# Optimization experiments

Measured on AMD Instinct MI355X. Metric: run time of the kernel, lower is better.

The kernel has to match this reference:

```python
import jax, jax.numpy as jnp
import numpy as np

RADIUS = 1.0
NSAMPLE = 32


def setup_inputs() -> dict:
    key = jax.random.key(0)
    k1, k2, k3, k4, k5 = jax.random.split(key, 5)
    B, Nb, M, K, C = 2, 2048, 64, 216, 32
    N = B * Nb
    # points in a 20m cube
    xyz = jax.random.uniform(k1, (N, 3), dtype=jnp.float32) * 20.0
    xyz_batch_cnt = jnp.array([Nb, Nb], dtype=jnp.int32)
    # rois: [x,y,z,dx,dy,dz,ry]
    ctr = jax.random.uniform(k2, (B, M, 3), dtype=jnp.float32) * 20.0
    dims = 1.0 + jax.random.uniform(k3, (B, M, 3), dtype=jnp.float32) * 2.0
    ry = jax.random.uniform(k4, (B, M, 1), dtype=jnp.float32) * 6.28
    rois = jnp.concatenate([ctr, dims, ry], axis=-1)
    # 6x6x6 grid points jittered around each roi center
    off = (jax.random.uniform(k5, (B, M, K, 3), dtype=jnp.float32) - 0.5) * 3.0
    new_xyz = ctr[:, :, None, :] + off
    features = jax.random.normal(jax.random.fold_in(key, 7), (N, C), dtype=jnp.float32)
    return {"xyz": xyz, "xyz_batch_cnt": xyz_batch_cnt, "new_xyz": new_xyz,
            "rois": rois, "features": features}


def _query_and_group(xyz, new_xyz, rois, features, B, Nb):
    """Ball query -> ragged compaction (padded to L=N*nsample) -> gather."""
    M, K = new_xyz.shape[1], new_xyz.shape[2]
    MK = M * K
    N = B * Nb
    L = N * NSAMPLE
    xyz_b = xyz.reshape(B, Nb, 3)
    grid = new_xyz.reshape(B, MK, 3)
    # squared distances point -> grid center, (B, Nb, MK)
    d2 = jnp.sum((xyz_b[:, :, None, :] - grid[:, None, :, :]) ** 2, axis=-1)
    # roi bounding sphere: center rois[:,:,:3], radius ||dims||_2 (the `ball` tensor)
    ctr = rois[:, :, :3]
    r2 = jnp.sum(rois[:, :, 3:6] ** 2, axis=-1)          # (B, M)
    d2b = jnp.sum((xyz_b[:, :, None, :] - ctr[:, None, :, :]) ** 2, axis=-1)  # (B,Nb,M)
    in_ball = (d2b <= r2[:, None, :])[:, :, :, None]      # (B,Nb,M,1)
    mask = (d2 <= RADIUS * RADIUS) & jnp.broadcast_to(in_ball, (B, Nb, M, K)).reshape(B, Nb, MK)
    # first-NSAMPLE-in-order selection per point (matches kernel iteration order)
    rank = jnp.cumsum(mask.astype(jnp.int32), axis=2) - 1
    cols = jnp.where(mask & (rank < NSAMPLE), rank, NSAMPLE)  # NSAMPLE = OOB -> dropped
    rows = jnp.broadcast_to(
        jnp.arange(B, dtype=jnp.int32)[:, None, None] * Nb
        + jnp.arange(Nb, dtype=jnp.int32)[None, :, None], (B, Nb, MK))
    flat_idx = jnp.broadcast_to(
        jnp.arange(B, dtype=jnp.int32)[:, None, None] * MK
        + jnp.arange(MK, dtype=jnp.int32)[None, None, :], (B, Nb, MK))
    ball_idx = jnp.full((N, NSAMPLE), -1, dtype=jnp.int32)
    ball_idx = ball_idx.at[rows.reshape(-1), cols.reshape(-1)].set(
        flat_idx.reshape(-1), mode="drop")
    # BallIndice: cumsum compaction of valid (point_idx, grid_idx) pairs, row-major
    valid = (ball_idx > -1).reshape(-1)                  # (L,)
    pos = jnp.cumsum(valid.astype(jnp.int32)) - 1
    pos_w = jnp.where(valid, pos, L)                     # invalid -> OOB -> dropped
    row_ids = jnp.broadcast_to(
        jnp.arange(N, dtype=jnp.int32)[:, None], (N, NSAMPLE)).reshape(-1)
    set_indices = jnp.zeros((L,), jnp.int32).at[pos_w].set(row_ids, mode="drop")
    set_new_indices = jnp.zeros((L,), jnp.int32).at[pos_w].set(
        ball_idx.reshape(-1), mode="drop")
    nind = jnp.sum(valid.astype(jnp.int32))
    vm = (jnp.arange(L) < nind)[:, None].astype(features.dtype)  # padding mask
    # GatherFeature (padded slots zeroed, matching new_zeros semantics)
    group_xyz = xyz[set_indices] * vm
    group_new_xyz = new_xyz.reshape(-1, 3)[set_new_indices] * vm
    group_feat = features[set_indices] * vm
    group_features = jnp.concatenate([group_xyz - group_new_xyz, group_feat], axis=1)
    return group_features, set_new_indices


def reference(xyz, xyz_batch_cnt, new_xyz, rois, features):
    B = xyz_batch_cnt.shape[0]
    Nb = xyz.shape[0] // B
    return _query_and_group(xyz, new_xyz, rois, features, B, Nb)
```

## Files before the change

kernel.cpp:

```cpp
#include <hip/hip_runtime.h>


#pragma clang fp contract(off)

typedef unsigned long long u64;

#define MAXN 4096

__global__ __launch_bounds__(256) void count_kernel(
    const float* __restrict__ xyz, const float* __restrict__ new_xyz,
    const float* __restrict__ rois, int* __restrict__ counts,
    int* __restrict__ ballidx, float* __restrict__ out_all,
    int N, int Nb, int M, int K, int nsample, int totalOut)
{
    __shared__ int plist[4][64];
    const int wave = threadIdx.x >> 6;
    const int lane = threadIdx.x & 63;
    const int r = blockIdx.x * 4 + wave;
    const u64 laneLt = (1ull << lane) - 1ull;

    {
        const int gtid = blockIdx.x * 256 + threadIdx.x;
        const int gthreads = gridDim.x * 256;
        for (int i = gtid; i < totalOut; i += gthreads) out_all[i] = 0.0f;
    }

    if (r >= N) return;

    const int b  = r / Nb;
    const float px = xyz[3 * r + 0];
    const float py = xyz[3 * r + 1];
    const float pz = xyz[3 * r + 2];

    bool pass = false;
    if (lane < M) {
        const float* rp = rois + (size_t)(b * M + lane) * 7;
        const float dx = rp[3], dy = rp[4], dz = rp[5];
        const float r2 = (dx * dx + dy * dy) + dz * dz;
        const float ex = px - rp[0], ey = py - rp[1], ez = pz - rp[2];
        pass = ((ex * ex + ey * ey) + ez * ez) <= r2;
    }
    const u64 roiMask = __ballot(pass);
    if (!roiMask) { if (lane == 0) counts[r] = 0; return; }
    if (pass) plist[wave][__popcll(roiMask & laneLt)] = lane;

    const int P = __popcll(roiMask);
    const int total = P * K;
    const float* nb_ = new_xyz + (size_t)(b * M * K) * 3;
    int* bi = ballidx + (size_t)r * nsample;

    int cnt = 0;
    for (int base = 0; base < total && cnt < nsample; base += 256) {
        bool match[4];
        int jj[4];
        #pragma unroll
        for (int u = 0; u < 4; u++) {
            const int p = base + u * 64 + lane;
            match[u] = false; jj[u] = 0;
            if (p < total) {
                const int ri = p / K;
                const int k  = p - ri * K;
                const int j  = plist[wave][ri] * K + k;
                jj[u] = j;
                const float* gp = nb_ + (size_t)j * 3;
                const float ax = px - gp[0], ay = py - gp[1], az = pz - gp[2];
                match[u] = ((ax * ax + ay * ay) + az * az) <= 1.0f;
            }
        }
        #pragma unroll
        for (int u = 0; u < 4; u++) {
            const u64 mm = __ballot(match[u]);
            const int slot = cnt + __popcll(mm & laneLt);
            if (match[u] && slot < nsample) bi[slot] = jj[u];
            cnt += __popcll(mm);
        }
    }
    if (lane == 0) counts[r] = cnt > nsample ? nsample : cnt;
}

__global__ __launch_bounds__(1024) void scan_kernel(
    const int* __restrict__ counts, int* __restrict__ offsets, int N)
{
    __shared__ int waveAux[16];
    const int t = threadIdx.x;
    const int lane = t & 63;
    const int wid = t >> 6;
    const int base = t * 4;
    int c[4];
    int s = 0;
    #pragma unroll
    for (int i = 0; i < 4; i++) {
        c[i] = (base + i < N) ? counts[base + i] : 0;
        s += c[i];
    }
    int incl = s;
    #pragma unroll
    for (int d = 1; d < 64; d <<= 1) {
        int v = __shfl_up(incl, d, 64);
        if (lane >= d) incl += v;
    }
    if (lane == 63) waveAux[wid] = incl;
    __syncthreads();
    if (t < 16) {
        int v = waveAux[t];
        #pragma unroll
        for (int d = 1; d < 16; d <<= 1) {
            int u = __shfl_up(v, d, 64);
            if (t >= d) v += u;
        }
        waveAux[t] = v;
    }
    __syncthreads();
    int run = (wid ? waveAux[wid - 1] : 0) + incl - s;
    #pragma unroll
    for (int i = 0; i < 4; i++) {
        if (base + i < N) offsets[base + i] = run;
        run += c[i];
    }
}

__global__ __launch_bounds__(256) void emit_kernel(
    const float* __restrict__ xyz, const float* __restrict__ new_xyz,
    const float* __restrict__ features,
    const int* __restrict__ counts, const int* __restrict__ offsets,
    const int* __restrict__ ballidx,
    float* __restrict__ out_feat, float* __restrict__ out_idx,
    int N, int Nb, int M, int K, int C, int nsample)
{
    const int wave = threadIdx.x >> 6;
    const int lane = threadIdx.x & 63;
    const int r = blockIdx.x * 4 + wave;
    if (r >= N) return;

    const int cnt = counts[r];
    if (cnt <= 0) return;

    const int b  = r / Nb;
    const int MK = M * K;
    const int obase = offsets[r];
    const int* bi = ballidx + (size_t)r * nsample;
    const float px = xyz[3 * r + 0];
    const float py = xyz[3 * r + 1];
    const float pz = xyz[3 * r + 2];
    const float* fr = features + (size_t)r * C;
    const float* nb_ = new_xyz + (size_t)b * MK * 3;
    const int W = 3 + C;

    float* dst = out_feat + (size_t)obase * W;
    const int tot = cnt * W;
    for (int idx = lane; idx < tot; idx += 64) {
        const int s = idx / W;
        const int c = idx - s * W;
        const int j = bi[s];
        float v;
        if (c == 0)      v = px - nb_[(size_t)j * 3 + 0];
        else if (c == 1) v = py - nb_[(size_t)j * 3 + 1];
        else if (c == 2) v = pz - nb_[(size_t)j * 3 + 2];
        else             v = fr[c - 3];
        dst[idx] = v;
    }
    for (int s = lane; s < cnt; s += 64)
        out_idx[obase + s] = (float)(b * MK + bi[s]);
}

extern "C" void kernel_launch(void* const* d_in, const int* in_sizes, int n_in,
                              void* d_out, int out_size, void* d_ws, size_t ws_size,
                              hipStream_t stream) {
    if (n_in < 5) return;

    int bc = 0;
    for (int i = 1; i < n_in; i++) if (in_sizes[i] < in_sizes[bc]) bc = i;
    const int B = in_sizes[bc];
    if (B < 1) return;

    int xi = -1, nwi = -1, ri = -1, fi = -1;
    int N = 0, M = 0, K = 0, C = 0, nsample = 0;

    for (int rr = 0; rr < n_in && xi < 0; rr++) {
        if (rr == bc) continue;
        if (in_sizes[rr] % (7 * B)) continue;
        const int M_ = in_sizes[rr] / (7 * B);
        if (M_ < 1 || M_ > 64) continue;
        for (int xx = 0; xx < n_in && xi < 0; xx++) {
            if (xx == bc || xx == rr) continue;
            if (in_sizes[xx] % 3) continue;
            const int N_ = in_sizes[xx] / 3;
            if (N_ < B || N_ % B || N_ > MAXN) continue;
            for (int nn = 0; nn < n_in && xi < 0; nn++) {
                if (nn == bc || nn == rr || nn == xx) continue;
                if (in_sizes[nn] % (3 * B * M_)) continue;
                const int K_ = in_sizes[nn] / (3 * B * M_);
                if (K_ < 1) continue;
                for (int ff = 0; ff < n_in && xi < 0; ff++) {
                    if (ff == bc || ff == rr || ff == xx || ff == nn) continue;
                    if (in_sizes[ff] % N_) continue;
                    const int C_ = in_sizes[ff] / N_;
                    if (C_ < 1) continue;
                    if (out_size % (4 + C_)) continue;
                    const long long L_ = (long long)out_size / (4 + C_);
                    if (L_ % N_) continue;
                    const int ns = (int)(L_ / N_);
                    if (ns < 1 || ns > 1024) continue;
                    xi = xx; nwi = nn; ri = rr; fi = ff;
                    N = N_; M = M_; K = K_; C = C_; nsample = ns;
                }
            }
        }
    }
    if (xi < 0) return;

    const float* xyz      = (const float*)d_in[xi];
    const float* new_xyz  = (const float*)d_in[nwi];
    const float* rois     = (const float*)d_in[ri];
    const float* features = (const float*)d_in[fi];
    const int Nb = N / B;

    const size_t L      = (size_t)N * nsample;
    const size_t chunk0 = L * (size_t)(3 + C);
    const int totalOut  = (int)(chunk0 + L);

    float* out_feat = (float*)d_out;
    float* out_idx  = out_feat + chunk0;

    const size_t wsNeed = ((size_t)2 * N + (size_t)N * nsample) * sizeof(int);
    if (ws_size < wsNeed) return;
    int* counts  = (int*)d_ws;
    int* offsets = counts + N;
    int* ballidx = offsets + N;

    const int blocks = (N + 3) / 4;

    count_kernel<<<blocks, 256, 0, stream>>>(
        xyz, new_xyz, rois, counts, ballidx, out_feat,
        N, Nb, M, K, nsample, totalOut);
    scan_kernel<<<1, 1024, 0, stream>>>(counts, offsets, N);
    emit_kernel<<<blocks, 256, 0, stream>>>(
        xyz, new_xyz, features, counts, offsets, ballidx,
        out_feat, out_idx, N, Nb, M, K, C, nsample);
}
```

Baseline: 91.73 us.

## Fold scan into emit via per-block sums and zero only the padded tail

Removes the separate single-block scan kernel. The count kernel now writes per-block totals, and each emit block reduces those totals redundantly to get its own prefix and the global count. The full-output zero fill moves out of the count kernel: the emit kernel now writes zeros only to the tail past the valid entries, using float4 stores. This cuts one launch and avoids writing the valid region twice, at the cost of every emit block re-reading all block sums.

```diff
diff --git a/kernel.cpp b/kernel.cpp
--- a/kernel.cpp
+++ b/kernel.cpp
@@ -10,157 +10,174 @@
 __global__ __launch_bounds__(256) void count_kernel(
     const float* __restrict__ xyz, const float* __restrict__ new_xyz,
     const float* __restrict__ rois, int* __restrict__ counts,
-    int* __restrict__ ballidx, float* __restrict__ out_all,
-    int N, int Nb, int M, int K, int nsample, int totalOut)
+    int* __restrict__ blockSums, int* __restrict__ ballidx,
+    int N, int Nb, int M, int K, int nsample)
 {
     __shared__ int plist[4][64];
+    __shared__ int scnt[4];
     const int wave = threadIdx.x >> 6;
     const int lane = threadIdx.x & 63;
     const int r = blockIdx.x * 4 + wave;
     const u64 laneLt = (1ull << lane) - 1ull;
 
-    {
-        const int gtid = blockIdx.x * 256 + threadIdx.x;
-        const int gthreads = gridDim.x * 256;
-        for (int i = gtid; i < totalOut; i += gthreads) out_all[i] = 0.0f;
-    }
-
-    if (r >= N) return;
-
-    const int b  = r / Nb;
-    const float px = xyz[3 * r + 0];
-    const float py = xyz[3 * r + 1];
-    const float pz = xyz[3 * r + 2];
-
-    bool pass = false;
-    if (lane < M) {
-        const float* rp = rois + (size_t)(b * M + lane) * 7;
-        const float dx = rp[3], dy = rp[4], dz = rp[5];
-        const float r2 = (dx * dx + dy * dy) + dz * dz;
-        const float ex = px - rp[0], ey = py - rp[1], ez = pz - rp[2];
-        pass = ((ex * ex + ey * ey) + ez * ez) <= r2;
-    }
-    const u64 roiMask = __ballot(pass);
-    if (!roiMask) { if (lane == 0) counts[r] = 0; return; }
-    if (pass) plist[wave][__popcll(roiMask & laneLt)] = lane;
-
-    const int P = __popcll(roiMask);
-    const int total = P * K;
-    const float* nb_ = new_xyz + (size_t)(b * M * K) * 3;
-    int* bi = ballidx + (size_t)r * nsample;
-
-    int cnt = 0;
-    for (int base = 0; base < total && cnt < nsample; base += 256) {
-        bool match[4];
-        int jj[4];
-        #pragma unroll
-        for (int u = 0; u < 4; u++) {
-            const int p = base + u * 64 + lane;
-            match[u] = false; jj[u] = 0;
-            if (p < total) {
-                const int ri = p / K;
-                const int k  = p - ri * K;
-                const int j  = plist[wave][ri] * K + k;
-                jj[u] = j;
-                const float* gp = nb_ + (size_t)j * 3;
-                const float ax = px - gp[0], ay = py - gp[1], az = pz - gp[2];
-                match[u] = ((ax * ax + ay * ay) + az * az) <= 1.0f;
-            }
-        }
-        #pragma unroll
-        for (int u = 0; u < 4; u++) {
-            const u64 mm = __ballot(match[u]);
-            const int slot = cnt + __popcll(mm & laneLt);
-            if (match[u] && slot < nsample) bi[slot] = jj[u];
-            cnt += __popcll(mm);
-        }
-    }
-    if (lane == 0) counts[r] = cnt > nsample ? nsample : cnt;
+    int cntc = 0;
+    if (r < N) {
+        const int b  = r / Nb;
+        const float px = xyz[3 * r + 0];
+        const float py = xyz[3 * r + 1];
+        const float pz = xyz[3 * r + 2];
+
+        bool pass = false;
+        if (lane < M) {
+            const float* rp = rois + (size_t)(b * M + lane) * 7;
+            const float dx = rp[3], dy = rp[4], dz = rp[5];
+            const float r2 = (dx * dx + dy * dy) + dz * dz;
+            const float ex = px - rp[0], ey = py - rp[1], ez = pz - rp[2];
+            pass = ((ex * ex + ey * ey) + ez * ez) <= r2;
+        }
+        const u64 roiMask = __ballot(pass);
+        if (roiMask) {
+            if (pass) plist[wave][__popcll(roiMask & laneLt)] = lane;
+
+            const int P = __popcll(roiMask);
+            const int total = P * K;
+            const float* nb_ = new_xyz + (size_t)(b * M * K) * 3;
+            int* bi = ballidx + (size_t)r * nsample;
+
+            int cnt = 0;
+            for (int base = 0; base < total && cnt < nsample; base += 256) {
+                bool match[4];
+                int jj[4];
+                #pragma unroll
+                for (int u = 0; u < 4; u++) {
+                    const int p = base + u * 64 + lane;
+                    match[u] = false; jj[u] = 0;
+                    if (p < total) {
+                        const int ri = p / K;
+                        const int k  = p - ri * K;
+                        const int j  = plist[wave][ri] * K + k;
+                        jj[u] = j;
+                        const float* gp = nb_ + (size_t)j * 3;
+                        const float ax = px - gp[0], ay = py - gp[1], az = pz - gp[2];
+                        match[u] = ((ax * ax + ay * ay) + az * az) <= 1.0f;
+                    }
+                }
+                #pragma unroll
+                for (int u = 0; u < 4; u++) {
+                    const u64 mm = __ballot(match[u]);
+                    const int slot = cnt + __popcll(mm & laneLt);
+                    if (match[u] && slot < nsample) bi[slot] = jj[u];
+                    cnt += __popcll(mm);
+                }
+            }
+            cntc = cnt > nsample ? nsample : cnt;
+        }
+        if (lane == 0) counts[r] = cntc;
+    }
+    if (lane == 0) scnt[wave] = cntc;
+    __syncthreads();
+    if (threadIdx.x == 0)
+        blockSums[blockIdx.x] = scnt[0] + scnt[1] + scnt[2] + scnt[3];
 }
 
-__global__ __launch_bounds__(1024) void scan_kernel(
-    const int* __restrict__ counts, int* __restrict__ offsets, int N)
+__global__ __launch_bounds__(256) void emit_kernel(
+    const float* __restrict__ xyz, const float* __restrict__ new_xyz,
+    const float* __restrict__ features,
+    const int* __restrict__ counts, const int* __restrict__ blockSums,
+    const int* __restrict__ ballidx,
+    float* __restrict__ out_feat, float* __restrict__ out_idx,
+    int N, int Nb, int M, int K, int C, int nsample, int numBlocks)
 {
-    __shared__ int waveAux[16];
+    __shared__ int sred[8];
     const int t = threadIdx.x;
     const int lane = t & 63;
     const int wid = t >> 6;
-    const int base = t * 4;
-    int c[4];
-    int s = 0;
-    #pragma unroll
-    for (int i = 0; i < 4; i++) {
-        c[i] = (base + i < N) ? counts[base + i] : 0;
-        s += c[i];
-    }
-    int incl = s;
-    #pragma unroll
-    for (int d = 1; d < 64; d <<= 1) {
-        int v = __shfl_up(incl, d, 64);
-        if (lane >= d) incl += v;
-    }
-    if (lane == 63) waveAux[wid] = incl;
+
+    int pre = 0, tot = 0;
+    {
+        const int b0 = t * 4;
+        #pragma unroll
+        for (int i = 0; i < 4; i++) {
+            const int bb = b0 + i;
+            if (bb < numBlocks) {
+                const int v = blockSums[bb];
+                tot += v;
+                if (bb < (int)blockIdx.x) pre += v;
+            }
+        }
+        #pragma unroll
+        for (int d = 1; d < 64; d <<= 1) {
+            pre += __shfl_xor(pre, d, 64);
+            tot += __shfl_xor(tot, d, 64);
+        }
+        if (lane == 0) { sred[wid] = pre; sred[4 + wid] = tot; }
+    }
     __syncthreads();
-    if (t < 16) {
-        int v = waveAux[t];
-        #pragma unroll
-        for (int d = 1; d < 16; d <<= 1) {
-            int u = __shfl_up(v, d, 64);
-            if (t >= d) v += u;
-        }
-        waveAux[t] = v;
-    }
-    __syncthreads();
-    int run = (wid ? waveAux[wid - 1] : 0) + incl - s;
-    #pragma unroll
-    for (int i = 0; i < 4; i++) {
-        if (base + i < N) offsets[base + i] = run;
-        run += c[i];
-    }
-}
-
-__global__ __launch_bounds__(256) void emit_kernel(
-    const float* __restrict__ xyz, const float* __restrict__ new_xyz,
-    const float* __restrict__ features,
-    const int* __restrict__ counts, const int* __restrict__ offsets,
-    const int* __restrict__ ballidx,
-    float* __restrict__ out_feat, float* __restrict__ out_idx,
-    int N, int Nb, int M, int K, int C, int nsample)
-{
-    const int wave = threadIdx.x >> 6;
-    const int lane = threadIdx.x & 63;
-    const int r = blockIdx.x * 4 + wave;
-    if (r >= N) return;
-
-    const int cnt = counts[r];
-    if (cnt <= 0) return;
-
-    const int b  = r / Nb;
-    const int MK = M * K;
-    const int obase = offsets[r];
-    const int* bi = ballidx + (size_t)r * nsample;
-    const float px = xyz[3 * r + 0];
-    const float py = xyz[3 * r + 1];
-    const float pz = xyz[3 * r + 2];
-    const float* fr = features + (size_t)r * C;
-    const float* nb_ = new_xyz + (size_t)b * MK * 3;
+    const int blockPre = sred[0] + sred[1] + sred[2] + sred[3];
+    const int nind     = sred[4] + sred[5] + sred[6] + sred[7];
+
     const int W = 3 + C;
-
-    float* dst = out_feat + (size_t)obase * W;
-    const int tot = cnt * W;
-    for (int idx = lane; idx < tot; idx += 64) {
-        const int s = idx / W;
-        const int c = idx - s * W;
-        const int j = bi[s];
-        float v;
-        if (c == 0)      v = px - nb_[(size_t)j * 3 + 0];
-        else if (c == 1) v = py - nb_[(size_t)j * 3 + 1];
-        else if (c == 2) v = pz - nb_[(size_t)j * 3 + 2];
-        else             v = fr[c - 3];
-        dst[idx] = v;
-    }
-    for (int s = lane; s < cnt; s += 64)
-        out_idx[obase + s] = (float)(b * MK + bi[s]);
+    const size_t L = (size_t)N * nsample;
+    const int r0 = blockIdx.x * 4;
+    const int r  = r0 + wid;
+
+    if (r < N) {
+        const int cnt = counts[r];
+        if (cnt > 0) {
+            int rowpre = 0;
+            if (lane < wid && (r0 + lane) < N) rowpre = counts[r0 + lane];
+            #pragma unroll
+            for (int d = 1; d < 64; d <<= 1) rowpre += __shfl_xor(rowpre, d, 64);
+
+            const int b  = r / Nb;
+            const int MK = M * K;
+            const int obase = blockPre + rowpre;
+            const int* bi = ballidx + (size_t)r * nsample;
+            const float px = xyz[3 * r + 0];
+            const float py = xyz[3 * r + 1];
+            const float pz = xyz[3 * r + 2];
+            const float* fr = features + (size_t)r * C;
+            const float* nb_ = new_xyz + (size_t)b * MK * 3;
+
+            float* dst = out_feat + (size_t)obase * W;
+            const int totE = cnt * W;
+            for (int idx = lane; idx < totE; idx += 64) {
+                const int s = idx / W;
+                const int c = idx - s * W;
+                const int j = bi[s];
+                float v;
+                if (c == 0)      v = px - nb_[(size_t)j * 3 + 0];
+                else if (c == 1) v = py - nb_[(size_t)j * 3 + 1];
+                else if (c == 2) v = pz - nb_[(size_t)j * 3 + 2];
+                else             v = fr[c - 3];
+                dst[idx] = v;
+            }
+            for (int s = lane; s < cnt; s += 64)
+                out_idx[obase + s] = (float)(b * MK + bi[s]);
+        }
+    }
+
+    const int gtid = blockIdx.x * 256 + t;
+    const int gthreads = gridDim.x * 256;
+    {
+        const size_t sA = (size_t)nind * W;
+        const size_t eA = L * (size_t)W;
+        if (sA < eA) {
+            const size_t s4 = (sA + 3) & ~(size_t)3;
+            const size_t headEnd = s4 < eA ? s4 : eA;
+            if ((size_t)gtid < headEnd - sA) out_feat[sA + gtid] = 0.0f;
+            if (s4 < eA) {
+                const size_t nvec = (eA - s4) >> 2;
+                float4* p4 = (float4*)(out_feat + s4);
+                const float4 z = make_float4(0.0f, 0.0f, 0.0f, 0.0f);
+                for (size_t i = gtid; i < nvec; i += gthreads) p4[i] = z;
+                const size_t rem = (eA - s4) & 3;
+                if ((size_t)gtid < rem) out_feat[eA - rem + gtid] = 0.0f;
+            }
+        }
+    }
+    for (size_t i = (size_t)nind + gtid; i < L; i += gthreads)
+        out_idx[i] = 0.0f;
 }
 
 extern "C" void kernel_launch(void* const* d_in, const int* in_sizes, int n_in,
@@ -217,24 +234,22 @@
 
     const size_t L      = (size_t)N * nsample;
     const size_t chunk0 = L * (size_t)(3 + C);
-    const int totalOut  = (int)(chunk0 + L);
 
     float* out_feat = (float*)d_out;
     float* out_idx  = out_feat + chunk0;
 
-    const size_t wsNeed = ((size_t)2 * N + (size_t)N * nsample) * sizeof(int);
+    const int blocks = (N + 3) / 4;
+
+    const size_t wsNeed = ((size_t)N + (size_t)blocks + (size_t)N * nsample) * sizeof(int);
     if (ws_size < wsNeed) return;
-    int* counts  = (int*)d_ws;
-    int* offsets = counts + N;
-    int* ballidx = offsets + N;
-
-    const int blocks = (N + 3) / 4;
+    int* counts    = (int*)d_ws;
+    int* blockSums = counts + N;
+    int* ballidx   = blockSums + blocks;
 
     count_kernel<<<blocks, 256, 0, stream>>>(
-        xyz, new_xyz, rois, counts, ballidx, out_feat,
-        N, Nb, M, K, nsample, totalOut);
-    scan_kernel<<<1, 1024, 0, stream>>>(counts, offsets, N);
+        xyz, new_xyz, rois, counts, blockSums, ballidx,
+        N, Nb, M, K, nsample);
     emit_kernel<<<blocks, 256, 0, stream>>>(
-        xyz, new_xyz, features, counts, offsets, ballidx,
-        out_feat, out_idx, N, Nb, M, K, C, nsample);
+        xyz, new_xyz, features, counts, blockSums, ballidx,
+        out_feat, out_idx, N, Nb, M, K, C, nsample, blocks);
 }
```

Measured after the change: 88.11 us. 3.9% less time.
